# Kernel optimization log

Measured on AMD Instinct MI355X. Metric: run time of the kernel, lower is better.

The kernel has to match this reference:

```python
import jax, jax.numpy as jnp
import numpy as np


def setup_inputs() -> dict:
    key = jax.random.key(0)
    kx, ks = jax.random.split(key)
    x = jax.random.normal(kx, (64, 128, 56, 56), dtype=jnp.float32)
    # scale must be nonnegative (asserted in torch forward); uniform (0,1)
    scale = jax.random.uniform(ks, (15,), dtype=jnp.float32, minval=0.05, maxval=1.0)
    return {
        "x": x,
        "scale": scale,
        "Qn": 0,
        "Qp": 15,
        "num_elements": 64 * 128 * 56 * 56,
        "box_size": 1024 * 256,
    }


def reference(x, scale, Qn, Qp, num_elements, box_size):
    # cumulative level boundaries (non-uniform quantization grid)
    cumsum_scale = jnp.cumsum(scale)                      # [Qp]
    # bucketize: midpoint boundaries (cumsum - scale/2), side='left' matches
    # torch.searchsorted(right=False)
    idx1 = jnp.searchsorted(cumsum_scale - scale * 0.5, x)  # [*x.shape]
    levels = jnp.concatenate([jnp.zeros((1,), x.dtype), cumsum_scale])  # [Qp+1]
    y = levels[idx1]
    return y
```

## Files before the change

### kernel.cpp

```cpp
#include <hip/hip_runtime.h>
#include <hip/hip_bf16.h>


__device__ __forceinline__ float quant_one(float x, const float* __restrict__ s,
                                           const float* __restrict__ b) {
    float acc = 0.0f;
#pragma unroll
    for (int j = 0; j < 15; ++j) {
        acc += (b[j] < x) ? s[j] : 0.0f;
    }
    return acc;
}

__global__ __launch_bounds__(256) void nulsq_quant_kernel(
    const float* __restrict__ x, const float* __restrict__ scale,
    float* __restrict__ y, int n4, int n) {
#pragma clang fp contract(off)
    float s[15], b[15];
    float c = 0.0f;
#pragma unroll
    for (int j = 0; j < 15; ++j) {
        s[j] = scale[j];
        c = c + s[j];
        b[j] = c - s[j] * 0.5f;
    }

    const float4* __restrict__ x4 = reinterpret_cast<const float4*>(x);
    float4* __restrict__ y4 = reinterpret_cast<float4*>(y);

    int tid = blockIdx.x * blockDim.x + threadIdx.x;
    int stride = gridDim.x * blockDim.x;

    for (int i = tid; i < n4; i += stride) {
        float4 v = x4[i];
        float4 r;
        r.x = quant_one(v.x, s, b);
        r.y = quant_one(v.y, s, b);
        r.z = quant_one(v.z, s, b);
        r.w = quant_one(v.w, s, b);
        y4[i] = r;
    }

    for (int i = n4 * 4 + tid; i < n; i += stride) {
        y[i] = quant_one(x[i], s, b);
    }
}

extern "C" void kernel_launch(void* const* d_in, const int* in_sizes, int n_in,
                              void* d_out, int out_size, void* d_ws, size_t ws_size,
                              hipStream_t stream) {
    const float* x = (const float*)d_in[0];
    const float* scale = (const float*)d_in[1];
    float* y = (float*)d_out;

    int n = in_sizes[0];
    int n4 = n / 4;

    const int block = 256;
    int grid = (n4 + block - 1) / block;
    if (grid > 2048) grid = 2048;
    if (grid < 1) grid = 1;

    nulsq_quant_kernel<<<grid, block, 0, stream>>>(x, scale, y, n4, n);
}
```

Baseline: 192.7 us.

## Replace grid-stride loop with fixed 4-vector-per-thread tiles and nontemporal stores

Drops the 2048-block grid-stride loop and launches one block per 1024 float4 vectors, with each thread issuing four independent 16-byte loads up front before computing. Outputs are written with nontemporal stores so the streaming result does not pollute cache, and the scalar tail is handled by block 0 only. The aim is more memory-level parallelism per thread and better cache behaviour on a bandwidth-bound elementwise kernel. The cost is a much larger grid, so per-block setup, including recomputing the 15 boundaries, is repeated more often.

New measurement: 189.4 us. About the same (-1.7%).

```diff
diff --git a/kernel.cpp b/kernel.cpp
--- a/kernel.cpp
+++ b/kernel.cpp
@@ -1,6 +1,8 @@
 #include <hip/hip_runtime.h>
 #include <hip/hip_bf16.h>
 
+
+typedef float vfloat4 __attribute__((ext_vector_type(4)));
 
 __device__ __forceinline__ float quant_one(float x, const float* __restrict__ s,
                                            const float* __restrict__ b) {
@@ -25,24 +27,39 @@
         b[j] = c - s[j] * 0.5f;
     }
 
-    const float4* __restrict__ x4 = reinterpret_cast<const float4*>(x);
-    float4* __restrict__ y4 = reinterpret_cast<float4*>(y);
+    const vfloat4* __restrict__ x4 = reinterpret_cast<const vfloat4*>(x);
+    vfloat4* __restrict__ y4 = reinterpret_cast<vfloat4*>(y);
 
-    int tid = blockIdx.x * blockDim.x + threadIdx.x;
-    int stride = gridDim.x * blockDim.x;
+    const int base = blockIdx.x * 1024 + (int)threadIdx.x;
 
-    for (int i = tid; i < n4; i += stride) {
-        float4 v = x4[i];
-        float4 r;
-        r.x = quant_one(v.x, s, b);
-        r.y = quant_one(v.y, s, b);
-        r.z = quant_one(v.z, s, b);
-        r.w = quant_one(v.w, s, b);
-        y4[i] = r;
+    vfloat4 v[4];
+    bool ok[4];
+    int fi[4];
+#pragma unroll
+    for (int k = 0; k < 4; ++k) {
+        fi[k] = base + k * 256;
+        ok[k] = fi[k] < n4;
+        if (ok[k]) v[k] = x4[fi[k]];
     }
 
-    for (int i = n4 * 4 + tid; i < n; i += stride) {
-        y[i] = quant_one(x[i], s, b);
+#pragma unroll
+    for (int k = 0; k < 4; ++k) {
+        if (ok[k]) {
+            vfloat4 r;
+            r.x = quant_one(v[k].x, s, b);
+            r.y = quant_one(v[k].y, s, b);
+            r.z = quant_one(v[k].z, s, b);
+            r.w = quant_one(v[k].w, s, b);
+            __builtin_nontemporal_store(r, &y4[fi[k]]);
+        }
+    }
+
+    if (blockIdx.x == 0) {
+        int tail = n - n4 * 4;
+        if ((int)threadIdx.x < tail) {
+            int i = n4 * 4 + (int)threadIdx.x;
+            y[i] = quant_one(x[i], s, b);
+        }
     }
 }
 
@@ -57,8 +74,8 @@
     int n4 = n / 4;
 
     const int block = 256;
-    int grid = (n4 + block - 1) / block;
-    if (grid > 2048) grid = 2048;
+    const int f4_per_block = block * 4;
+    int grid = (n4 + f4_per_block - 1) / f4_per_block;
     if (grid < 1) grid = 1;
 
     nulsq_quant_kernel<<<grid, block, 0, stream>>>(x, scale, y, n4, n);
```
